# Kernel tuning notes

Hardware: AMD Instinct MI355X
Metric: run time of the kernel (lower is better)

Reference implementation:

```python
import jax, jax.numpy as jnp
import numpy as np


def conv1x1(x, W, b):
    # 1x1 Conv2d == per-pixel linear over channels. x: [B,C,H,W], W: [O,C], b: [O]
    return jnp.einsum('oc,bchw->bohw', W, x) + b[None, :, None, None]


def setup_inputs() -> dict:
    key = jax.random.key(0)
    ks = jax.random.split(key, 18)
    B, C, Hd, H, W = 16, 64, 64, 32, 32
    s = 0.05
    f = jax.random.normal
    return {
        'h': f(ks[0], (B, C, H, W), jnp.float32),
        'm': f(ks[1], (B, C, H, W), jnp.float32),
        'Wq': f(ks[2], (Hd, C), jnp.float32) * s,
        'bq': f(ks[3], (Hd,), jnp.float32) * s,
        'Wk': f(ks[4], (Hd, C), jnp.float32) * s,
        'bk': f(ks[5], (Hd,), jnp.float32) * s,
        'Wk2': f(ks[6], (Hd, C), jnp.float32) * s,
        'bk2': f(ks[7], (Hd,), jnp.float32) * s,
        'Wv': f(ks[8], (C, C), jnp.float32) * s,
        'bv': f(ks[9], (C,), jnp.float32) * s,
        'Wv2': f(ks[10], (C, C), jnp.float32) * s,
        'bv2': f(ks[11], (C,), jnp.float32) * s,
        'Wz': f(ks[12], (2 * C, 2 * C), jnp.float32) * s,
        'bz': f(ks[13], (2 * C,), jnp.float32) * s,
        'Wm': f(ks[14], (3 * C, 3 * C), jnp.float32) * s,
        'bm': f(ks[15], (3 * C,), jnp.float32) * s,
    }


def reference(h, m, Wq, bq, Wk, bk, Wk2, bk2, Wv, bv, Wv2, bv2, Wz, bz, Wm, bm):
    B, C, H, W = h.shape
    Hd = Wq.shape[0]
    N = H * W
    # Shared query from h
    Q_h = conv1x1(h, Wq, bq).reshape(B, Hd, N).transpose(0, 2, 1)  # [B,N,Hd]
    # Self-attention branch over h
    K_h = conv1x1(h, Wk, bk).reshape(B, Hd, N)                     # [B,Hd,N]
    A_h = jax.nn.softmax(jnp.einsum('bnd,bdm->bnm', Q_h, K_h), axis=-1)  # [B,N,N]
    V_h = conv1x1(h, Wv, bv).reshape(B, C, N)                      # [B,C,N]
    Z_h = jnp.einsum('bnm,bcm->bcn', A_h, V_h).reshape(B, C, H, W)
    # Cross-attention branch over memory m (same query Q_h)
    K_m = conv1x1(m, Wk2, bk2).reshape(B, Hd, N)
    A_m = jax.nn.softmax(jnp.einsum('bnd,bdm->bnm', Q_h, K_m), axis=-1)
    V_m = conv1x1(m, Wv2, bv2).reshape(B, C, N)
    Z_m = jnp.einsum('bnm,bcm->bcn', A_m, V_m).reshape(B, C, H, W)
    # Fuse and gated memory update
    Z = conv1x1(jnp.concatenate([Z_h, Z_m], axis=1), Wz, bz)       # [B,2C,H,W]
    combined = conv1x1(jnp.concatenate([Z, h], axis=1), Wm, bm)    # [B,3C,H,W]
    mo, mg, mi = combined[:, :C], combined[:, C:2 * C], combined[:, 2 * C:]
    mi = jax.nn.sigmoid(mi)
    new_m = (1 - mi) * m + mi * jnp.tanh(mg)
    new_h = jax.nn.sigmoid(mo) * new_m
    return (new_h, new_m)
```

## Files before the change

### kernel.cpp

```cpp
#include <hip/hip_runtime.h>

typedef unsigned short u16;
typedef unsigned int u32;
typedef __attribute__((ext_vector_type(8))) short bf16x8;
typedef __attribute__((ext_vector_type(4))) short bf16x4;
typedef __attribute__((ext_vector_type(4))) float f32x4;

#define MFMA(a, b, c) __builtin_amdgcn_mfma_f32_16x16x32_bf16((a), (b), (c), 0, 0, 0)
#define MFMA16(a, b, c) __builtin_amdgcn_mfma_f32_16x16x16bf16_1k((a), (b), (c), 0, 0, 0)

static __device__ __forceinline__ u16 f2bf(float x) {
  u32 u = __float_as_uint(x);
  u += 0x7FFFu + ((u >> 16) & 1u);
  return (u16)(u >> 16);
}
static __device__ __forceinline__ u32 packbf_t(float hi, float lo) {
  return __builtin_amdgcn_perm(__float_as_uint(hi), __float_as_uint(lo), 0x07060302u);
}
static __device__ __forceinline__ u32 packbf(float lo, float hi) {
  return (u32)f2bf(lo) | ((u32)f2bf(hi) << 16);
}

__global__ __launch_bounds__(256) void proj_kernel(
    const float* __restrict__ h, const float* __restrict__ m_,
    const float* __restrict__ bq, const float* __restrict__ bk,
    const float* __restrict__ bk2, const float* __restrict__ bv,
    const float* __restrict__ bv2,
    const float* __restrict__ Wq, const float* __restrict__ Wk,
    const float* __restrict__ Wk2, const float* __restrict__ Wv,
    const float* __restrict__ Wv2,
    const float* __restrict__ Wz, const float* __restrict__ Wm,
    const float* __restrict__ bm,
    u16* __restrict__ Qb, u16* __restrict__ Khb, u16* __restrict__ Kmb,
    u16* __restrict__ Vhb, u16* __restrict__ Vmb, u16* __restrict__ hbuf,
    u16* __restrict__ Wzb, u16* __restrict__ Wmb, float* __restrict__ bmp)
{
  const int tid = threadIdx.x;
  const int b = blockIdx.y, n0 = blockIdx.x * 64, z = blockIdx.z;

  {
    const int gid = (blockIdx.z * 256 + blockIdx.y * 16 + blockIdx.x) * 256 + tid;
    if (gid < 16384) {
      Wzb[gid] = f2bf(Wz[gid]);
    } else if (gid < 53248) {
      const int e = gid - 16384;
      const int p = e / 192, k = e % 192;
      const int hb2 = p / 96, r1 = p % 96, ctl = r1 / 48, r2 = r1 % 48;
      const int g = r2 >> 4, mm = r2 & 15;
      const int o = g * 64 + (hb2 * 2 + ctl) * 16 + mm;
      Wmb[p * 192 + k] = f2bf(Wm[o * 192 + k]);
    } else if (gid < 53440) {
      const int p = gid - 53248;
      const int hb2 = p / 96, r1 = p % 96, ctl = r1 / 48, r2 = r1 % 48;
      const int g = r2 >> 4, mm = r2 & 15;
      const int o = g * 64 + (hb2 * 2 + ctl) * 16 + mm;
      bmp[p] = bm[o];
    }
  }

  __shared__ __align__(16) u16 xt[64][72];
  const float* __restrict__ X = z ? m_ : h;

  {
    const int px = tid & 63, c0 = (tid >> 6) * 16;
#pragma unroll
    for (int i = 0; i < 8; ++i) {
      const int c = c0 + 2 * i;
      const float f0 = X[(b * 64 + c) * 1024 + n0 + px];
      const float f1 = X[(b * 64 + c + 1) * 1024 + n0 + px];
      *(u32*)&xt[px][c] = packbf(f0, f1);
    }
  }
  __syncthreads();

  const int lane = tid & 63, w = tid >> 6;
  const int mm = lane & 15, q = lane >> 4;

  const bf16x8 xa0 = *(const bf16x8*)&xt[w * 16 + mm][q * 8];
  const bf16x8 xa1 = *(const bf16x8*)&xt[w * 16 + mm][32 + q * 8];

  auto ldw8 = [&](const float* Wf, int row, int col0) {
    const float4 a = *(const float4*)(Wf + row * 64 + col0);
    const float4 bb = *(const float4*)(Wf + row * 64 + col0 + 4);
    union { u32 u[4]; bf16x8 v; } r;
    r.u[0] = packbf(a.x, a.y);
    r.u[1] = packbf(a.z, a.w);
    r.u[2] = packbf(bb.x, bb.y);
    r.u[3] = packbf(bb.z, bb.w);
    return r.v;
  };

  auto qk_store = [&](u16* dst, const float* Wf, const float* bias) {
#pragma unroll
    for (int ot = 0; ot < 4; ++ot) {
      const bf16x8 wb0 = ldw8(Wf, ot * 16 + mm, q * 8);
      const bf16x8 wb1 = ldw8(Wf, ot * 16 + mm, 32 + q * 8);
      const float4 b4 = *(const float4*)(bias + ot * 16 + q * 4);
      f32x4 d = {b4.x, b4.y, b4.z, b4.w};
      d = MFMA(wb0, xa0, d);
      d = MFMA(wb1, xa1, d);
      uint2 val;
      val.x = packbf(d[0], d[1]);
      val.y = packbf(d[2], d[3]);
      *(uint2*)(dst + (b * 1024 + n0 + w * 16 + mm) * 64 + ot * 16 + q * 4) = val;
    }
  };
  auto v_store = [&](u16* dst, const float* Wf, const float* bias) {
#pragma unroll
    for (int ot = 0; ot < 4; ++ot) {
      const bf16x8 wb0 = ldw8(Wf, ot * 16 + mm, q * 8);
      const bf16x8 wb1 = ldw8(Wf, ot * 16 + mm, 32 + q * 8);
      const float bb = bias[ot * 16 + mm];
      f32x4 d = {bb, bb, bb, bb};
      d = MFMA(xa0, wb0, d);
      d = MFMA(xa1, wb1, d);
      uint2 val;
      val.x = packbf(d[0], d[1]);
      val.y = packbf(d[2], d[3]);
      *(uint2*)(dst + b * 65536 + blockIdx.x * 4096 + (ot * 16 + mm) * 64 +
                w * 16 + q * 4) = val;
    }
  };

  if (z == 0) {
    qk_store(Qb, Wq, bq);
    qk_store(Khb, Wk, bk);
    v_store(Vhb, Wv, bv);
    const int px = tid >> 2, sg = tid & 3;
    u32* dst = (u32*)(hbuf + (b * 1024 + n0 + px) * 64 + sg * 16);
    const u16* srcr = &xt[px][sg * 16];
#pragma unroll
    for (int j = 0; j < 8; ++j) dst[j] = *(const u32*)(srcr + 2 * j);
  } else {
    qk_store(Kmb, Wk2, bk2);
    v_store(Vmb, Wv2, bv2);
  }
}

__global__ __launch_bounds__(256, 4) void attn_kernel(
    const u16* __restrict__ Qb, const u16* __restrict__ Khb,
    const u16* __restrict__ Kmb, const u16* __restrict__ Vhb,
    const u16* __restrict__ Vmb, u16* __restrict__ Ztb)
{
  const int id = blockIdx.x;
  const int b = id & 15;
  const int br = (id >> 4) & 1;
  const int qh = id >> 5;
  const u16* __restrict__ K = (br ? Kmb : Khb) + b * 65536;
  const u16* __restrict__ V = (br ? Vmb : Vhb) + b * 65536;

  __shared__ __align__(16) u16 pool[18432];
  __shared__ float rsw[4][32];
  u16* const Kl = pool;
  u16* const Vl = pool + 9216;

  const int tid = threadIdx.x, w = tid >> 6, lane = tid & 63;
  const int mm = lane & 15, q = lane >> 4;
  const int q0 = qh * 32;

  bf16x8 qb0[2], qb1[2];
#pragma unroll
  for (int qt = 0; qt < 2; ++qt) {
    const u16* Qp = Qb + (b * 1024 + q0 + qt * 16 + mm) * 64;
    qb0[qt] = *(const bf16x8*)(Qp + q * 8);
    qb1[qt] = *(const bf16x8*)(Qp + 32 + q * 8);
  }

  f32x4 z[2][4];
#pragma unroll
  for (int qt = 0; qt < 2; ++qt)
#pragma unroll
    for (int ct = 0; ct < 4; ++ct) z[qt][ct] = (f32x4){0.f, 0.f, 0.f, 0.f};
  float rp[2] = {0.f, 0.f};

  const int so0 = (tid >> 3) * 72 + (tid & 7) * 8;
  const int so1 = so0 + 32 * 72;
  uint4 sk0, sk1, sv0, sv1;
  auto stage_load = [&](int kc) {
    const u16* Ks = K + kc * 4096;
    const u16* Vs = V + kc * 4096;
    sk0 = *(const uint4*)(Ks + tid * 8);
    sk1 = *(const uint4*)(Ks + tid * 8 + 2048);
    sv0 = *(const uint4*)(Vs + tid * 8);
    sv1 = *(const uint4*)(Vs + tid * 8 + 2048);
  };
  auto stage_store = [&](int buf) {
    u16* Kd = Kl + buf * 4608;
    u16* Vd = Vl + buf * 4608;
    *(uint4*)(Kd + so0) = sk0;
    *(uint4*)(Kd + so1) = sk1;
    *(uint4*)(Vd + so0) = sv0;
    *(uint4*)(Vd + so1) = sv1;
  };

  stage_load(0);
  stage_store(0);
  __syncthreads();

  int cur = 0;
#pragma unroll 1
  for (int kc = 0; kc < 16; ++kc) {
    if (kc < 15) stage_load(kc + 1);

    const u16* Kc = Kl + cur * 4608;
    const u16* Vc = Vl + cur * 4608;
    const bf16x8 kf0 = *(const bf16x8*)(Kc + (w * 16 + mm) * 72 + q * 8);
    const bf16x8 kf1 = *(const bf16x8*)(Kc + (w * 16 + mm) * 72 + 32 + q * 8);
    bf16x4 vf[4];
#pragma unroll
    for (int ct = 0; ct < 4; ++ct)
      vf[ct] = *(const bf16x4*)(Vc + (ct * 16 + mm) * 72 + w * 16 + q * 4);

#pragma unroll
    for (int qt = 0; qt < 2; ++qt) {
      f32x4 s = {0.f, 0.f, 0.f, 0.f};
      s = MFMA(kf0, qb0[qt], s);
      s = MFMA(kf1, qb1[qt], s);
      const float e0 = __expf(s[0]), e1 = __expf(s[1]);
      const float e2 = __expf(s[2]), e3 = __expf(s[3]);
      rp[qt] += (e0 + e1) + (e2 + e3);
      union { u32 u[2]; bf16x4 v; } pb;
      pb.u[0] = packbf_t(e1, e0);
      pb.u[1] = packbf_t(e3, e2);
#pragma unroll
      for (int ct = 0; ct < 4; ++ct) z[qt][ct] = MFMA16(vf[ct], pb.v, z[qt][ct]);
    }

    if (kc < 15) stage_store(cur ^ 1);
    __syncthreads();
    cur ^= 1;
  }

  u16* const zcb = pool;
#pragma unroll
  for (int qt = 0; qt < 2; ++qt) {
    float v = rp[qt];
    v += __shfl_xor(v, 16);
    v += __shfl_xor(v, 32);
    if (q == 0) rsw[w][qt * 16 + mm] = v;
#pragma unroll
    for (int ct = 0; ct < 4; ++ct) {
      uint2 val;
      val.x = packbf_t(z[qt][ct][1], z[qt][ct][0]);
      val.y = packbf_t(z[qt][ct][3], z[qt][ct][2]);
      *(uint2*)(zcb + w * 2176 + (qt * 16 + mm) * 68 + ct * 16 + q * 4) = val;
    }
  }
  __syncthreads();

  const int c2 = tid & 31, qr = tid >> 5;
#pragma unroll
  for (int i = 0; i < 4; ++i) {
    const int query = qr + i * 8;
    const float rt = rsw[0][query] + rsw[1][query] + rsw[2][query] + rsw[3][query];
    const float rinv = __builtin_amdgcn_rcpf(rt);
    float vlo = 0.f, vhi = 0.f;
#pragma unroll
    for (int ww = 0; ww < 4; ++ww) {
      const u32 u = *(const u32*)(zcb + ww * 2176 + query * 68 + c2 * 2);
      vlo += __uint_as_float(u << 16);
      vhi += __uint_as_float(u & 0xffff0000u);
    }
    vlo *= rinv;
    vhi *= rinv;
    *(u32*)(Ztb + (b * 1024 + q0 + query) * 128 + br * 64 + c2 * 2) = packbf_t(vhi, vlo);
  }
}

__global__ __launch_bounds__(256) void tail_kernel(
    const u16* __restrict__ Ztb, const u16* __restrict__ hbuf,
    const float* __restrict__ m_, const u16* __restrict__ Wzb,
    const float* __restrict__ bz, const u16* __restrict__ Wmb,
    const float* __restrict__ bmp, float* __restrict__ out)
{
  const int b = blockIdx.y, n0 = blockIdx.x * 32;
  __shared__ __align__(16) u16 zp[32][136];
  const int tid = threadIdx.x, lane = tid & 63, wv = tid >> 6;
  const int mm = lane & 15, q = lane >> 4;
  const int pxt = wv & 1, oh = wv >> 1;

  {
    bf16x8 za[4];
#pragma unroll
    for (int ks = 0; ks < 4; ++ks)
      za[ks] = *(const bf16x8*)(Ztb + (b * 1024 + n0 + pxt * 16 + mm) * 128 +
                                ks * 32 + q * 8);
#pragma unroll
    for (int ot = 0; ot < 4; ++ot) {
      const int o0 = oh * 64 + ot * 16;
      const float4 b4 = *(const float4*)(bz + o0 + q * 4);
      f32x4 d = {b4.x, b4.y, b4.z, b4.w};
#pragma unroll
      for (int ks = 0; ks < 4; ++ks) {
        const bf16x8 wb = *(const bf16x8*)(Wzb + (o0 + mm) * 128 + ks * 32 + q * 8);
        d = MFMA(wb, za[ks], d);
      }
      uint2 val;
      val.x = packbf(d[0], d[1]);
      val.y = packbf(d[2], d[3]);
      *(uint2*)&zp[pxt * 16 + mm][o0 + q * 4] = val;
    }
  }
  __syncthreads();

  {
    const int hb2 = oh;
    bf16x8 fa[6];
#pragma unroll
    for (int ks = 0; ks < 4; ++ks)
      fa[ks] = *(const bf16x8*)&zp[pxt * 16 + mm][ks * 32 + q * 8];
    {
      const u16* hp = hbuf + (b * 1024 + n0 + pxt * 16 + mm) * 64;
      fa[4] = *(const bf16x8*)(hp + q * 8);
      fa[5] = *(const bf16x8*)(hp + 32 + q * 8);
    }
    f32x4 dd[6];
#pragma unroll
    for (int j = 0; j < 6; ++j) {
      const int p = hb2 * 96 + j * 16 + mm;
      const float bb = bmp[p];
      f32x4 d = {bb, bb, bb, bb};
#pragma unroll
      for (int ks = 0; ks < 6; ++ks) {
        const bf16x8 wb = *(const bf16x8*)(Wmb + p * 192 + ks * 32 + q * 8);
        d = MFMA(fa[ks], wb, d);
      }
      dd[j] = d;
    }
#pragma unroll
    for (int ctl = 0; ctl < 2; ++ctl) {
      const int c = (hb2 * 2 + ctl) * 16 + mm;
      const int px = n0 + pxt * 16 + q * 4;
      const float4 mold = *(const float4*)(m_ + (b * 64 + c) * 1024 + px);
      float4 nh, nm;
#pragma unroll
      for (int r = 0; r < 4; ++r) {
        const float xo = dd[ctl * 3 + 0][r];
        const float xg = dd[ctl * 3 + 1][r];
        const float xi = dd[ctl * 3 + 2][r];
        const float si = __builtin_amdgcn_rcpf(1.f + __expf(-xi));
        const float th = 1.f - 2.f * __builtin_amdgcn_rcpf(__expf(2.f * xg) + 1.f);
        const float so = __builtin_amdgcn_rcpf(1.f + __expf(-xo));
        const float mo = ((const float*)&mold)[r];
        const float nmv = (1.f - si) * mo + si * th;
        ((float*)&nm)[r] = nmv;
        ((float*)&nh)[r] = so * nmv;
      }
      *(float4*)(out + (b * 64 + c) * 1024 + px) = nh;
      *(float4*)(out + 1048576 + (b * 64 + c) * 1024 + px) = nm;
    }
  }
}

extern "C" void kernel_launch(void* const* d_in, const int* in_sizes, int n_in,
                              void* d_out, int out_size, void* d_ws, size_t ws_size,
                              hipStream_t stream) {
  const float* h   = (const float*)d_in[0];
  const float* m   = (const float*)d_in[1];
  const float* Wq  = (const float*)d_in[2];
  const float* bq  = (const float*)d_in[3];
  const float* Wk  = (const float*)d_in[4];
  const float* bk  = (const float*)d_in[5];
  const float* Wk2 = (const float*)d_in[6];
  const float* bk2 = (const float*)d_in[7];
  const float* Wv  = (const float*)d_in[8];
  const float* bv  = (const float*)d_in[9];
  const float* Wv2 = (const float*)d_in[10];
  const float* bv2 = (const float*)d_in[11];
  const float* Wz  = (const float*)d_in[12];
  const float* bz  = (const float*)d_in[13];
  const float* Wm  = (const float*)d_in[14];
  const float* bm  = (const float*)d_in[15];
  float* out = (float*)d_out;

  char* ws = (char*)d_ws;
  const size_t MB = 1024 * 1024;
  u16* Qb   = (u16*)(ws + 0 * MB);
  u16* Khb  = (u16*)(ws + 2 * MB);
  u16* Kmb  = (u16*)(ws + 4 * MB);
  u16* Vhb  = (u16*)(ws + 6 * MB);
  u16* Vmb  = (u16*)(ws + 8 * MB);
  u16* hbuf = (u16*)(ws + 10 * MB);
  u16* Ztb  = (u16*)(ws + 12 * MB);
  u16* Wzb  = (u16*)(ws + 16 * MB + 40960);
  u16* Wmb  = (u16*)(ws + 16 * MB + 73728);
  float* bmp = (float*)(ws + 16 * MB + 147456);

  proj_kernel<<<dim3(16, 16, 2), 256, 0, stream>>>(
      h, m, bq, bk, bk2, bv, bv2, Wq, Wk, Wk2, Wv, Wv2, Wz, Wm, bm,
      Qb, Khb, Kmb, Vhb, Vmb, hbuf, Wzb, Wmb, bmp);
  attn_kernel<<<1024, 256, 0, stream>>>(Qb, Khb, Kmb, Vhb, Vmb, Ztb);
  tail_kernel<<<dim3(32, 16), 256, 0, stream>>>(Ztb, hbuf, m, Wzb, bz, Wmb, bmp, out);
}
```

Measured before the change: 140.0 us.

## Split projection and tail kernels into more blocks for higher parallelism

The projection kernel grid grows from 2 to 5 z-slices so that each block computes a single projection (Q, K_h, V_h, K_m, V_m) rather than two or three. The tail kernel processes 16 pixels per block instead of 32, doubling its grid to 1024 blocks, with each wave owning one channel slice. Both changes aim to fill more compute units on a small problem, at the cost of reloading and converting the input tile redundantly across blocks and reloading the weights more often. The weight-preparation path keyed on global id may now also run in the extra z-slices, depending on how gid is formed.

```diff
diff --git a/kernel.cpp b/kernel.cpp
--- a/kernel.cpp
+++ b/kernel.cpp
@@ -59,7 +59,7 @@
   }
 
   __shared__ __align__(16) u16 xt[64][72];
-  const float* __restrict__ X = z ? m_ : h;
+  const float* __restrict__ X = (z >= 3) ? m_ : h;
 
   {
     const int px = tid & 63, c0 = (tid >> 6) * 16;
@@ -124,15 +124,18 @@
 
   if (z == 0) {
     qk_store(Qb, Wq, bq);
-    qk_store(Khb, Wk, bk);
-    v_store(Vhb, Wv, bv);
     const int px = tid >> 2, sg = tid & 3;
     u32* dst = (u32*)(hbuf + (b * 1024 + n0 + px) * 64 + sg * 16);
     const u16* srcr = &xt[px][sg * 16];
 #pragma unroll
     for (int j = 0; j < 8; ++j) dst[j] = *(const u32*)(srcr + 2 * j);
+  } else if (z == 1) {
+    qk_store(Khb, Wk, bk);
+  } else if (z == 2) {
+    v_store(Vhb, Wv, bv);
+  } else if (z == 3) {
+    qk_store(Kmb, Wk2, bk2);
   } else {
-    qk_store(Kmb, Wk2, bk2);
     v_store(Vmb, Wv2, bv2);
   }
 }
@@ -273,21 +276,19 @@
     const float* __restrict__ bz, const u16* __restrict__ Wmb,
     const float* __restrict__ bmp, float* __restrict__ out)
 {
-  const int b = blockIdx.y, n0 = blockIdx.x * 32;
-  __shared__ __align__(16) u16 zp[32][136];
+  const int b = blockIdx.y, n0 = blockIdx.x * 16;
+  __shared__ __align__(16) u16 zp[16][136];
   const int tid = threadIdx.x, lane = tid & 63, wv = tid >> 6;
   const int mm = lane & 15, q = lane >> 4;
-  const int pxt = wv & 1, oh = wv >> 1;
 
   {
     bf16x8 za[4];
 #pragma unroll
     for (int ks = 0; ks < 4; ++ks)
-      za[ks] = *(const bf16x8*)(Ztb + (b * 1024 + n0 + pxt * 16 + mm) * 128 +
-                                ks * 32 + q * 8);
-#pragma unroll
-    for (int ot = 0; ot < 4; ++ot) {
-      const int o0 = oh * 64 + ot * 16;
+      za[ks] = *(const bf16x8*)(Ztb + (b * 1024 + n0 + mm) * 128 + ks * 32 + q * 8);
+#pragma unroll
+    for (int ot = 0; ot < 2; ++ot) {
+      const int o0 = wv * 32 + ot * 16;
       const float4 b4 = *(const float4*)(bz + o0 + q * 4);
       f32x4 d = {b4.x, b4.y, b4.z, b4.w};
 #pragma unroll
@@ -298,26 +299,25 @@
       uint2 val;
       val.x = packbf(d[0], d[1]);
       val.y = packbf(d[2], d[3]);
-      *(uint2*)&zp[pxt * 16 + mm][o0 + q * 4] = val;
+      *(uint2*)&zp[mm][o0 + q * 4] = val;
     }
   }
   __syncthreads();
 
   {
-    const int hb2 = oh;
     bf16x8 fa[6];
 #pragma unroll
     for (int ks = 0; ks < 4; ++ks)
-      fa[ks] = *(const bf16x8*)&zp[pxt * 16 + mm][ks * 32 + q * 8];
+      fa[ks] = *(const bf16x8*)&zp[mm][ks * 32 + q * 8];
     {
-      const u16* hp = hbuf + (b * 1024 + n0 + pxt * 16 + mm) * 64;
+      const u16* hp = hbuf + (b * 1024 + n0 + mm) * 64;
       fa[4] = *(const bf16x8*)(hp + q * 8);
       fa[5] = *(const bf16x8*)(hp + 32 + q * 8);
     }
-    f32x4 dd[6];
-#pragma unroll
-    for (int j = 0; j < 6; ++j) {
-      const int p = hb2 * 96 + j * 16 + mm;
+    f32x4 dd[3];
+#pragma unroll
+    for (int j = 0; j < 3; ++j) {
+      const int p = wv * 48 + j * 16 + mm;
       const float bb = bmp[p];
       f32x4 d = {bb, bb, bb, bb};
 #pragma unroll
@@ -327,28 +327,25 @@
       }
       dd[j] = d;
     }
-#pragma unroll
-    for (int ctl = 0; ctl < 2; ++ctl) {
-      const int c = (hb2 * 2 + ctl) * 16 + mm;
-      const int px = n0 + pxt * 16 + q * 4;
-      const float4 mold = *(const float4*)(m_ + (b * 64 + c) * 1024 + px);
-      float4 nh, nm;
-#pragma unroll
-      for (int r = 0; r < 4; ++r) {
-        const float xo = dd[ctl * 3 + 0][r];
-        const float xg = dd[ctl * 3 + 1][r];
-        const float xi = dd[ctl * 3 + 2][r];
-        const float si = __builtin_amdgcn_rcpf(1.f + __expf(-xi));
-        const float th = 1.f - 2.f * __builtin_amdgcn_rcpf(__expf(2.f * xg) + 1.f);
-        const float so = __builtin_amdgcn_rcpf(1.f + __expf(-xo));
-        const float mo = ((const float*)&mold)[r];
-        const float nmv = (1.f - si) * mo + si * th;
-        ((float*)&nm)[r] = nmv;
-        ((float*)&nh)[r] = so * nmv;
-      }
-      *(float4*)(out + (b * 64 + c) * 1024 + px) = nh;
-      *(float4*)(out + 1048576 + (b * 64 + c) * 1024 + px) = nm;
-    }
+    const int c = wv * 16 + mm;
+    const int px = n0 + q * 4;
+    const float4 mold = *(const float4*)(m_ + (b * 64 + c) * 1024 + px);
+    float4 nh, nm;
+#pragma unroll
+    for (int r = 0; r < 4; ++r) {
+      const float xo = dd[0][r];
+      const float xg = dd[1][r];
+      const float xi = dd[2][r];
+      const float si = __builtin_amdgcn_rcpf(1.f + __expf(-xi));
+      const float th = 1.f - 2.f * __builtin_amdgcn_rcpf(__expf(2.f * xg) + 1.f);
+      const float so = __builtin_amdgcn_rcpf(1.f + __expf(-xo));
+      const float mo = ((const float*)&mold)[r];
+      const float nmv = (1.f - si) * mo + si * th;
+      ((float*)&nm)[r] = nmv;
+      ((float*)&nh)[r] = so * nmv;
+    }
+    *(float4*)(out + (b * 64 + c) * 1024 + px) = nh;
+    *(float4*)(out + 1048576 + (b * 64 + c) * 1024 + px) = nm;
   }
 }
 
@@ -386,9 +383,9 @@
   u16* Wmb  = (u16*)(ws + 16 * MB + 73728);
   float* bmp = (float*)(ws + 16 * MB + 147456);
 
-  proj_kernel<<<dim3(16, 16, 2), 256, 0, stream>>>(
+  proj_kernel<<<dim3(16, 16, 5), 256, 0, stream>>>(
       h, m, bq, bk, bk2, bv, bv2, Wq, Wk, Wk2, Wv, Wv2, Wz, Wm, bm,
       Qb, Khb, Kmb, Vhb, Vmb, hbuf, Wzb, Wmb, bmp);
   attn_kernel<<<1024, 256, 0, stream>>>(Qb, Khb, Kmb, Vhb, Vmb, Ztb);
-  tail_kernel<<<dim3(32, 16), 256, 0, stream>>>(Ztb, hbuf, m, Wzb, bz, Wmb, bmp, out);
-}
+  tail_kernel<<<dim3(64, 16), 256, 0, stream>>>(Ztb, hbuf, m, Wzb, bz, Wmb, bmp, out);
+}
```

New measurement: 138.5 us. Within noise of the previous version (-1.1%).
